# Performance work log

Measured on AMD Instinct MI355X. Metric: run time of the kernel, lower is better.

Reference implementation:

```python
import jax, jax.numpy as jnp
import numpy as np
import math

B, C_IN, C_OUT, K, STYLE_DIM, H, W = 16, 512, 512, 3, 512, 64, 64
EPS = 1e-8
CONV_SCALE = 1.0 / math.sqrt(C_IN * K * K)   # fan_in scale in ModulatedConv2d
MOD_SCALE = 1.0 / math.sqrt(STYLE_DIM)       # EqualLinear scale (lr_mul=1)


def setup_inputs() -> dict:
    key = jax.random.key(0)
    k1, k2, k3, k4 = jax.random.split(key, 4)
    inp = {
        "input": jax.random.normal(k1, (B, C_IN, H, W), dtype=jnp.float32),
        "style": jax.random.normal(k2, (B, STYLE_DIM), dtype=jnp.float32),
        # learned params
        "conv_weight": jax.random.normal(k3, (1, C_OUT, C_IN, K, K), dtype=jnp.float32),
        "mod_weight": jax.random.normal(k4, (C_IN, STYLE_DIM), dtype=jnp.float32),
        "mod_bias": jnp.ones((C_IN,), dtype=jnp.float32),  # bias_init=1
    }
    return inp


def reference(input, style, conv_weight, mod_weight, mod_bias):
    # EqualLinear modulation: style_mod[b, c_in]
    s = style @ (mod_weight * MOD_SCALE).T + mod_bias  # [B, C_in]
    # per-sample modulated weight: [B, C_out, C_in, K, K]
    w = CONV_SCALE * conv_weight * s[:, None, :, None, None]
    # demodulation
    demod = jax.lax.rsqrt(jnp.sum(w * w, axis=(2, 3, 4)) + EPS)  # [B, C_out]
    w = w * demod[:, :, None, None, None]
    # per-sample conv2d with 'same' padding (pad = K // 2), equivalent to groups=batch
    pad = K // 2

    def conv_one(x, wk):
        # x: [C_in, H, W], wk: [C_out, C_in, K, K]
        return jax.lax.conv_general_dilated(
            x[None], wk, window_strides=(1, 1),
            padding=[(pad, pad), (pad, pad)],
            dimension_numbers=("NCHW", "OIHW", "NCHW"))[0]

    out = jax.vmap(conv_one)(input, w)  # [B, C_out, H, W]
    return out
```

## Files before the change

### kernel.cpp

```cpp
#include <hip/hip_runtime.h>
#include <cstdint>
#include <cstddef>

#define BATCH 16
#define CIN 512
#define COUT 512
#define STYLE_D 512
#define EPSC 1e-8f
#define CONV_SCALE_F 0.014731391274719739f
#define MOD_SCALE_F  0.04419417382415922f

typedef __attribute__((ext_vector_type(8))) short bhalf8;
typedef __attribute__((ext_vector_type(4))) float f32x4;

__device__ __forceinline__ unsigned short f2bf(float f){
  unsigned int u = __float_as_uint(f);
  u += 0x7fffu + ((u >> 16) & 1u);
  return (unsigned short)(u >> 16);
}

__device__ __forceinline__ void load_lds16(const void* g, void* l){
  __builtin_amdgcn_global_load_lds(
      (const __attribute__((address_space(1))) uint32_t*)g,
      (__attribute__((address_space(3))) uint32_t*)l, 16, 0, 0);
}

__global__ void k_style(const float* __restrict__ style, const float* __restrict__ mw,
                        const float* __restrict__ mb, float* __restrict__ a){
  int t = blockIdx.x * 256 + threadIdx.x;
  int b = t >> 9, c = t & 511;
  const float4* s4 = (const float4*)(style + b * STYLE_D);
  const float4* w4 = (const float4*)(mw + (size_t)c * STYLE_D);
  float s = 0.f;
#pragma unroll 4
  for (int k = 0; k < STYLE_D / 4; ++k){
    float4 sv = s4[k], wv = w4[k];
    s += sv.x * wv.x + sv.y * wv.y + sv.z * wv.z + sv.w * wv.w;
  }
  s = s * MOD_SCALE_F + mb[c];
  a[t] = CONV_SCALE_F * s;
}

__global__ void k_wprep(const float* __restrict__ cw, float* __restrict__ r,
                        unsigned short* __restrict__ W2){
  int t = blockIdx.x * 256 + threadIdx.x;
  int co = t >> 9, ci = t & 511;
  const float* w = cw + (size_t)t * 9;
  float acc = 0.f; float v[9];
#pragma unroll
  for (int j = 0; j < 9; ++j){ v[j] = w[j]; acc += v[j] * v[j]; }
  r[t] = acc;
#pragma unroll
  for (int tap = 0; tap < 9; ++tap)
    W2[((size_t)tap * COUT + co) * CIN + ci] = f2bf(v[tap]);
}

__global__ void k_demod(const float* __restrict__ a, const float* __restrict__ r,
                        float* __restrict__ d){
  int t = blockIdx.x * 256 + threadIdx.x;
  int b = t >> 9, co = t & 511;
  const float4* a4 = (const float4*)(a + b * CIN);
  const float4* r4 = (const float4*)(r + (size_t)co * CIN);
  float s = 0.f;
#pragma unroll 4
  for (int k = 0; k < CIN / 4; ++k){
    float4 av = a4[k], rv = r4[k];
    s += av.x*av.x*rv.x + av.y*av.y*rv.y + av.z*av.z*rv.z + av.w*av.w*rv.w;
  }
  d[t] = rsqrtf(s + EPSC);
}

__global__ void k_xprep(const float* __restrict__ in, const float* __restrict__ a,
                        unsigned short* __restrict__ x2){
  __shared__ float tile[32][65];
  int bx = blockIdx.x;
  int b  = bx >> 10;
  int ct = (bx >> 6) & 15;
  int pt = bx & 63;
  int c0 = ct * 32, p0 = pt * 64;
  int t = threadIdx.x;
  int xx = t & 63, c4 = t >> 6;
  const float* src = in + ((size_t)b * CIN + c0) * 4096 + p0;
#pragma unroll
  for (int i = 0; i < 8; ++i){
    int cl = i * 4 + c4;
    tile[cl][xx] = src[(size_t)cl * 4096 + xx];
  }
  __syncthreads();
  int c = t & 31, p4 = t >> 5;
  float av = a[b * CIN + c0 + c];
  unsigned short* dst = x2 + ((size_t)b * 4096 + p0) * CIN + c0 + c;
#pragma unroll
  for (int i = 0; i < 8; ++i){
    int pl = i * 8 + p4;
    dst[(size_t)pl * CIN] = f2bf(av * tile[c][pl]);
  }
}

#define NSLOT_IN 1344
#define NCHUNK 57
__global__ __launch_bounds__(256, 2) void k_conv(
    const unsigned short* __restrict__ x2, const unsigned short* __restrict__ W2,
    const float* __restrict__ d, const char* __restrict__ zp,
    float* __restrict__ out){
  __shared__ __align__(16) unsigned char smem[(NSLOT_IN + 2304) * 16];

  int bx = blockIdx.x;
  int b   = bx >> 7;
  int rem = bx & 127;
  int coT = rem >> 4;
  int pt  = rem & 15;
  int y0 = (pt >> 2) * 16, x0 = (pt & 3) * 16;

  int tid = threadIdx.x, lane = tid & 63, w = tid >> 6;

  const int nch = (w == 0) ? 15 : 14;
  const char* ga[15];
#pragma unroll
  for (int i = 0; i < 15; ++i){
    if (i < nch){
      int ch = i * 4 + w;
      int slot = ch * 64 + lane;
      const char* p;
      if (slot < 1296){
        int c = slot / 324;
        int r2 = slot - c * 324;
        int iy = r2 / 18, ix = r2 - iy * 18;
        int gy = y0 + iy - 1, gx = x0 + ix - 1;
        if (gy >= 0 && gy < 64 && gx >= 0 && gx < 64)
          p = (const char*)x2 + (((size_t)b * 4096 + gy * 64 + gx) * CIN + c * 8) * 2;
        else
          p = zp;
      } else if (slot < NSLOT_IN){
        p = zp;
      } else {
        int sw = slot - NSLOT_IN;
        int tap = sw >> 8, r2 = sw & 255, q = r2 >> 6, co = r2 & 63;
        p = (const char*)W2 + (((size_t)tap * COUT + coT * 64 + co) * CIN + q * 8) * 2;
      }
      ga[i] = p;
    }
  }

  const int q = lane >> 4, n = lane & 15;
  const unsigned int bBase = (unsigned)(q * 324 + n) * 16u;
  const unsigned int aBase = (unsigned)(NSLOT_IN + q * 64 + n) * 16u;

  f32x4 acc[4][4];
#pragma unroll
  for (int cf = 0; cf < 4; ++cf)
#pragma unroll
    for (int pf = 0; pf < 4; ++pf)
      acc[cf][pf] = (f32x4){0.f, 0.f, 0.f, 0.f};

  for (int s = 0; s < 16; ++s){
#pragma unroll
    for (int i = 0; i < 15; ++i){
      if (i < nch){
        int ch = i * 4 + w;
        load_lds16(ga[i], smem + ch * 1024 + lane * 16);
        ga[i] += 64;
      }
    }
    __syncthreads();
#pragma unroll
    for (int tap = 0; tap < 9; ++tap){
      const int ki = tap / 3, kj = tap - ki * 3;
      bhalf8 av[4];
#pragma unroll
      for (int cf = 0; cf < 4; ++cf)
        av[cf] = *(const bhalf8*)(smem + aBase + (unsigned)(tap * 256 + cf * 16) * 16u);
#pragma unroll
      for (int pf = 0; pf < 4; ++pf){
        unsigned boff = bBase + (unsigned)(((w * 4 + pf + ki) * 18 + kj) * 16);
        bhalf8 bv = *(const bhalf8*)(smem + boff);
#pragma unroll
        for (int cf = 0; cf < 4; ++cf)
          acc[cf][pf] = __builtin_amdgcn_mfma_f32_16x16x32_bf16(av[cf], bv, acc[cf][pf], 0, 0, 0);
      }
    }
    __syncthreads();
  }

  const float* dp = d + b * COUT;
  int rowq = (lane >> 4) * 4;
#pragma unroll
  for (int cf = 0; cf < 4; ++cf){
#pragma unroll
    for (int r = 0; r < 4; ++r){
      int co = coT * 64 + cf * 16 + rowq + r;
      float dv = dp[co];
      float* op = out + (((size_t)b * COUT + co) * 64 + y0 + w * 4) * 64 + x0 + n;
#pragma unroll
      for (int pf = 0; pf < 4; ++pf)
        op[(size_t)pf * 64] = dv * acc[cf][pf][r];
    }
  }
}

__global__ void k_demod_direct(const float* __restrict__ a, const float* __restrict__ cw,
                               float* __restrict__ d){
  int t = blockIdx.x * 256 + threadIdx.x;
  int b = t & 15, co = t >> 4;
  const float* ar = a + b * CIN;
  const float* wr = cw + (size_t)co * CIN * 9;
  float s = 0.f;
  for (int ci = 0; ci < CIN; ++ci){
    float av = ar[ci], rr = 0.f;
#pragma unroll
    for (int j = 0; j < 9; ++j){ float v = wr[ci * 9 + j]; rr += v * v; }
    s += av * av * rr;
  }
  d[b * COUT + co] = rsqrtf(s + EPSC);
}

__global__ void k_conv_naive(const float* __restrict__ in, const float* __restrict__ cw,
                             const float* __restrict__ a, const float* __restrict__ d,
                             float* __restrict__ out){
  size_t t = (size_t)blockIdx.x * 256 + threadIdx.x;
  int x = t & 63, y = (t >> 6) & 63;
  int co = (t >> 12) & 511, b = (int)(t >> 21);
  const float* ar = a + b * CIN;
  const float* wr = cw + (size_t)co * CIN * 9;
  const float* ib = in + (size_t)b * CIN * 4096;
  float acc = 0.f;
  for (int ci = 0; ci < CIN; ++ci){
    float av = ar[ci];
    const float* ip = ib + (size_t)ci * 4096;
    const float* wp = wr + ci * 9;
#pragma unroll
    for (int dy = 0; dy < 3; ++dy){
      int gy = y + dy - 1;
      if (gy < 0 || gy > 63) continue;
#pragma unroll
      for (int dx = 0; dx < 3; ++dx){
        int gx = x + dx - 1;
        if (gx < 0 || gx > 63) continue;
        acc += wp[dy * 3 + dx] * av * ip[gy * 64 + gx];
      }
    }
  }
  out[t] = d[b * COUT + co] * acc;
}

extern "C" void kernel_launch(void* const* d_in, const int* in_sizes, int n_in,
                              void* d_out, int out_size, void* d_ws, size_t ws_size,
                              hipStream_t stream){
  (void)in_sizes; (void)n_in; (void)out_size;
  const float* in    = (const float*)d_in[0];
  const float* style = (const float*)d_in[1];
  const float* cw    = (const float*)d_in[2];
  const float* mw    = (const float*)d_in[3];
  const float* mb    = (const float*)d_in[4];
  float* out = (float*)d_out;

  char* ws = (char*)d_ws;
  const size_t ZP_OFF = 0;
  const size_t A_OFF  = 4096;
  const size_t D_OFF  = A_OFF + 32768;
  const size_t R_OFF  = D_OFF + 32768;
  const size_t W2_OFF = R_OFF + 1048576;
  const size_t X2_OFF = W2_OFF + (size_t)9 * COUT * CIN * 2;
  const size_t WS_NEED = X2_OFF + (size_t)BATCH * 4096 * CIN * 2;

  float* a    = (float*)(ws + A_OFF);
  float* dmod = (float*)(ws + D_OFF);

  if (ws_size >= WS_NEED){
    float* r = (float*)(ws + R_OFF);
    unsigned short* W2 = (unsigned short*)(ws + W2_OFF);
    unsigned short* x2 = (unsigned short*)(ws + X2_OFF);
    hipMemsetAsync(ws + ZP_OFF, 0, 4096, stream);
    k_style<<<32, 256, 0, stream>>>(style, mw, mb, a);
    k_wprep<<<1024, 256, 0, stream>>>(cw, r, W2);
    k_demod<<<32, 256, 0, stream>>>(a, r, dmod);
    k_xprep<<<16384, 256, 0, stream>>>(in, a, x2);
    k_conv<<<2048, 256, 0, stream>>>(x2, W2, dmod, ws + ZP_OFF, out);
  } else {
    k_style<<<32, 256, 0, stream>>>(style, mw, mb, a);
    k_demod_direct<<<32, 256, 0, stream>>>(a, cw, dmod);
    k_conv_naive<<<131072, 256, 0, stream>>>(in, cw, a, dmod, out);
  }
}
```

Measured before the change: 557.4 us.

## Switch conv to 32x32x16 MFMA with larger pixel tiles and packed xprep stores

The implicit-GEMM conv kernel moves from 16x16x32 to 32x32x16 bf16 MFMAs. Each block now covers a 16x32 pixel tile per 64 output channels, so there are half as many blocks and each stage loads 16 input channels over 32 stages. The activation halo is reused across more pixels and there are fewer A/B fragment loads per FLOP. The xprep transpose now handles 64 channels per image row and writes packed bf16 pairs as 32-bit stores to cut store count. The trade-off is 128 accumulator registers per thread and twice as many barrier-synchronised stages with smaller per-stage loads, which may hurt latency hiding.

```diff
diff --git a/kernel.cpp b/kernel.cpp
--- a/kernel.cpp
+++ b/kernel.cpp
@@ -11,7 +11,7 @@
 #define MOD_SCALE_F  0.04419417382415922f
 
 typedef __attribute__((ext_vector_type(8))) short bhalf8;
-typedef __attribute__((ext_vector_type(4))) float f32x4;
+typedef __attribute__((ext_vector_type(16))) float f32x16;
 
 __device__ __forceinline__ unsigned short f2bf(float f){
   unsigned int u = __float_as_uint(f);
@@ -70,130 +70,117 @@
   d[t] = rsqrtf(s + EPSC);
 }
 
-__global__ void k_xprep(const float* __restrict__ in, const float* __restrict__ a,
-                        unsigned short* __restrict__ x2){
-  __shared__ float tile[32][65];
+__global__ __launch_bounds__(256) void k_xprep(const float* __restrict__ in,
+                                               const float* __restrict__ a,
+                                               unsigned short* __restrict__ x2){
+  __shared__ float tile[64][67];
   int bx = blockIdx.x;
-  int b  = bx >> 10;
-  int ct = (bx >> 6) & 15;
-  int pt = bx & 63;
-  int c0 = ct * 32, p0 = pt * 64;
-  int t = threadIdx.x;
-  int xx = t & 63, c4 = t >> 6;
-  const float* src = in + ((size_t)b * CIN + c0) * 4096 + p0;
-#pragma unroll
-  for (int i = 0; i < 8; ++i){
+  int b = bx >> 9, cgrp = (bx >> 6) & 7, y = bx & 63;
+  int c0 = cgrp * 64;
+  int tid = threadIdx.x;
+  int xx = tid & 63, c4 = tid >> 6;
+  const float* src = in + ((size_t)(b * CIN + c0)) * 4096 + y * 64;
+#pragma unroll
+  for (int i = 0; i < 16; ++i){
     int cl = i * 4 + c4;
     tile[cl][xx] = src[(size_t)cl * 4096 + xx];
   }
   __syncthreads();
-  int c = t & 31, p4 = t >> 5;
-  float av = a[b * CIN + c0 + c];
-  unsigned short* dst = x2 + ((size_t)b * 4096 + p0) * CIN + c0 + c;
+  int cg = tid & 31;
+  float a0 = a[b * CIN + c0 + cg * 2];
+  float a1 = a[b * CIN + c0 + cg * 2 + 1];
+  unsigned int* dst = (unsigned int*)(x2 + ((size_t)(b * 4096 + y * 64)) * CIN + c0);
 #pragma unroll
   for (int i = 0; i < 8; ++i){
-    int pl = i * 8 + p4;
-    dst[(size_t)pl * CIN] = f2bf(av * tile[c][pl]);
-  }
-}
-
-#define NSLOT_IN 1344
-#define NCHUNK 57
+    int px = i * 8 + (tid >> 5);
+    float v0 = tile[cg * 2][px], v1 = tile[cg * 2 + 1][px];
+    unsigned int pack = (unsigned int)f2bf(a0 * v0) | ((unsigned int)f2bf(a1 * v1) << 16);
+    dst[(size_t)px * (CIN / 2) + cg] = pack;
+  }
+}
+
+#define LDS_W_BASE 19584
+#define NCHUNK_TOT 2376
 __global__ __launch_bounds__(256, 2) void k_conv(
     const unsigned short* __restrict__ x2, const unsigned short* __restrict__ W2,
-    const float* __restrict__ d, const char* __restrict__ zp,
+    const float* __restrict__ dmod, const char* __restrict__ zp,
     float* __restrict__ out){
-  __shared__ __align__(16) unsigned char smem[(NSLOT_IN + 2304) * 16];
+  __shared__ __align__(16) unsigned char smem[2560 * 16];
 
   int bx = blockIdx.x;
-  int b   = bx >> 7;
-  int rem = bx & 127;
-  int coT = rem >> 4;
-  int pt  = rem & 15;
-  int y0 = (pt >> 2) * 16, x0 = (pt & 3) * 16;
-
+  int b = bx >> 6, coT = (bx >> 3) & 7, pt = bx & 7;
+  int y0 = (pt >> 1) * 16, x0 = (pt & 1) * 32;
   int tid = threadIdx.x, lane = tid & 63, w = tid >> 6;
 
-  const int nch = (w == 0) ? 15 : 14;
-  const char* ga[15];
-#pragma unroll
-  for (int i = 0; i < 15; ++i){
-    if (i < nch){
-      int ch = i * 4 + w;
-      int slot = ch * 64 + lane;
-      const char* p;
-      if (slot < 1296){
-        int c = slot / 324;
-        int r2 = slot - c * 324;
-        int iy = r2 / 18, ix = r2 - iy * 18;
-        int gy = y0 + iy - 1, gx = x0 + ix - 1;
-        if (gy >= 0 && gy < 64 && gx >= 0 && gx < 64)
-          p = (const char*)x2 + (((size_t)b * 4096 + gy * 64 + gx) * CIN + c * 8) * 2;
-        else
-          p = zp;
-      } else if (slot < NSLOT_IN){
-        p = zp;
-      } else {
-        int sw = slot - NSLOT_IN;
-        int tap = sw >> 8, r2 = sw & 255, q = r2 >> 6, co = r2 & 63;
-        p = (const char*)W2 + (((size_t)tap * COUT + coT * 64 + co) * CIN + q * 8) * 2;
-      }
-      ga[i] = p;
-    }
-  }
-
-  const int q = lane >> 4, n = lane & 15;
-  const unsigned int bBase = (unsigned)(q * 324 + n) * 16u;
-  const unsigned int aBase = (unsigned)(NSLOT_IN + q * 64 + n) * 16u;
-
-  f32x4 acc[4][4];
-#pragma unroll
-  for (int cf = 0; cf < 4; ++cf)
-#pragma unroll
-    for (int pf = 0; pf < 4; ++pf)
-      acc[cf][pf] = (f32x4){0.f, 0.f, 0.f, 0.f};
-
-  for (int s = 0; s < 16; ++s){
-#pragma unroll
-    for (int i = 0; i < 15; ++i){
-      if (i < nch){
-        int ch = i * 4 + w;
-        load_lds16(ga[i], smem + ch * 1024 + lane * 16);
-        ga[i] += 64;
-      }
+  const char* ga[10];
+#pragma unroll
+  for (int i = 0; i < 10; ++i){
+    int chunk = i * 256 + tid;
+    const char* p;
+    if (chunk < 1224){
+      int pix = chunk >> 1, kh = chunk & 1;
+      int iy = pix / 34, ix = pix - iy * 34;
+      int gy = y0 + iy - 1, gx = x0 + ix - 1;
+      if (gy >= 0 && gy < 64 && gx >= 0 && gx < 64)
+        p = (const char*)x2 + (((size_t)(b * 4096 + gy * 64 + gx)) * CIN + kh * 8) * 2;
+      else p = zp;
+    } else if (chunk < NCHUNK_TOT){
+      int sw = chunk - 1224;
+      int tap = sw >> 7, cf = (sw >> 6) & 1, kh = (sw >> 5) & 1, co = sw & 31;
+      p = (const char*)W2 + (((size_t)(tap * COUT + coT * 64 + cf * 32 + co)) * CIN + kh * 8) * 2;
+    } else {
+      p = zp;
+    }
+    ga[i] = p;
+  }
+
+  f32x16 acc[2][4];
+#pragma unroll
+  for (int cf = 0; cf < 2; ++cf)
+#pragma unroll
+    for (int nf = 0; nf < 4; ++nf)
+#pragma unroll
+      for (int e = 0; e < 16; ++e) acc[cf][nf][e] = 0.f;
+
+  const unsigned bvLane = (unsigned)((lane & 31) * 32 + (lane >> 5) * 16);
+  const unsigned char* wbase = smem + LDS_W_BASE + lane * 16;
+  const unsigned wrow = (unsigned)(w * 4);
+
+  for (int s = 0; s < 32; ++s){
+#pragma unroll
+    for (int i = 0; i < 10; ++i){
+      load_lds16(ga[i], smem + (i * 256 + tid) * 16);
+      ga[i] += 32;
     }
     __syncthreads();
 #pragma unroll
     for (int tap = 0; tap < 9; ++tap){
       const int ki = tap / 3, kj = tap - ki * 3;
-      bhalf8 av[4];
-#pragma unroll
-      for (int cf = 0; cf < 4; ++cf)
-        av[cf] = *(const bhalf8*)(smem + aBase + (unsigned)(tap * 256 + cf * 16) * 16u);
-#pragma unroll
-      for (int pf = 0; pf < 4; ++pf){
-        unsigned boff = bBase + (unsigned)(((w * 4 + pf + ki) * 18 + kj) * 16);
-        bhalf8 bv = *(const bhalf8*)(smem + boff);
-#pragma unroll
-        for (int cf = 0; cf < 4; ++cf)
-          acc[cf][pf] = __builtin_amdgcn_mfma_f32_16x16x32_bf16(av[cf], bv, acc[cf][pf], 0, 0, 0);
+      bhalf8 a0 = *(const bhalf8*)(wbase + tap * 2048);
+      bhalf8 a1 = *(const bhalf8*)(wbase + tap * 2048 + 1024);
+#pragma unroll
+      for (int nf = 0; nf < 4; ++nf){
+        bhalf8 bv = *(const bhalf8*)(smem + ((wrow + nf + ki) * 34 + kj) * 32 + bvLane);
+        acc[0][nf] = __builtin_amdgcn_mfma_f32_32x32x16_bf16(a0, bv, acc[0][nf], 0, 0, 0);
+        acc[1][nf] = __builtin_amdgcn_mfma_f32_32x32x16_bf16(a1, bv, acc[1][nf], 0, 0, 0);
       }
     }
     __syncthreads();
   }
 
-  const float* dp = d + b * COUT;
-  int rowq = (lane >> 4) * 4;
-#pragma unroll
-  for (int cf = 0; cf < 4; ++cf){
-#pragma unroll
-    for (int r = 0; r < 4; ++r){
-      int co = coT * 64 + cf * 16 + rowq + r;
-      float dv = dp[co];
-      float* op = out + (((size_t)b * COUT + co) * 64 + y0 + w * 4) * 64 + x0 + n;
-#pragma unroll
-      for (int pf = 0; pf < 4; ++pf)
-        op[(size_t)pf * 64] = dv * acc[cf][pf][r];
+  int n = lane & 31, kh = lane >> 5;
+  const float* dp = dmod + b * COUT + coT * 64;
+#pragma unroll
+  for (int cf = 0; cf < 2; ++cf){
+#pragma unroll
+    for (int nf = 0; nf < 4; ++nf){
+      int gy = y0 + w * 4 + nf;
+      float* orow = out + ((size_t)(b * COUT + coT * 64 + cf * 32)) * 4096 + gy * 64 + x0 + n;
+#pragma unroll
+      for (int reg = 0; reg < 16; ++reg){
+        int row = (reg & 3) + 8 * (reg >> 2) + 4 * kh;
+        orow[(size_t)row * 4096] = dp[cf * 32 + row] * acc[cf][nf][reg];
+      }
     }
   }
 }
@@ -274,8 +261,8 @@
     k_style<<<32, 256, 0, stream>>>(style, mw, mb, a);
     k_wprep<<<1024, 256, 0, stream>>>(cw, r, W2);
     k_demod<<<32, 256, 0, stream>>>(a, r, dmod);
-    k_xprep<<<16384, 256, 0, stream>>>(in, a, x2);
-    k_conv<<<2048, 256, 0, stream>>>(x2, W2, dmod, ws + ZP_OFF, out);
+    k_xprep<<<8192, 256, 0, stream>>>(in, a, x2);
+    k_conv<<<1024, 256, 0, stream>>>(x2, W2, dmod, ws + ZP_OFF, out);
   } else {
     k_style<<<32, 256, 0, stream>>>(style, mw, mb, a);
     k_demod_direct<<<32, 256, 0, stream>>>(a, cw, dmod);
```

Measured after the change: 527.7 us. 5.3% less time.
